# Optimization experiments

Measured on AMD Instinct MI355X. Metric: run time of the kernel, lower is better.

The kernel has to match this reference:

```python
import jax, jax.numpy as jnp
import numpy as np


def _block_causal_mask(cu_seqlens, seq_len):
    """Boolean [seq_len, seq_len] mask: True = attend (same doc AND causal)."""
    positions = jnp.arange(seq_len)
    # searchsorted(side='right') - 1 maps each position to its document id
    seq_ids = jnp.searchsorted(cu_seqlens, positions, side='right') - 1
    same_seq = seq_ids[:, None] == seq_ids[None, :]
    causal = positions[None, :] <= positions[:, None]
    return same_seq & causal


def setup_inputs() -> dict:
    key = jax.random.key(0)
    kq, kk, kv, kc = jax.random.split(key, 4)
    B, H, S, D = 1, 16, 4096, 128
    q = jax.random.normal(kq, (B, H, S, D), dtype=jnp.float32)
    k = jax.random.normal(kk, (B, H, S, D), dtype=jnp.float32)
    v = jax.random.normal(kv, (B, H, S, D), dtype=jnp.float32)
    # 8 packed documents: interior boundaries are sorted random ints in (0, S)
    inner = jnp.sort(jax.random.randint(kc, (7,), 1, S, dtype=jnp.int64))
    cu_seqlens = jnp.concatenate([
        jnp.zeros((1,), jnp.int64), inner, jnp.full((1,), S, jnp.int64)
    ])
    return {"q": q, "k": k, "v": v, "cu_seqlens": cu_seqlens, "max_seqlen": S}


def reference(q, k, v, cu_seqlens, max_seqlen):
    # q, k, v: [B, H, S, D]; block-diagonal causal SDPA over packed sequences.
    S, D = q.shape[2], q.shape[3]
    scale = 1.0 / jnp.sqrt(jnp.asarray(D, q.dtype))
    allow = _block_causal_mask(cu_seqlens, S)  # [S, S] bool
    scores = jnp.einsum('bhsd,bhtd->bhst', q, k) * scale  # [B, H, S, S]
    neg_inf = jnp.asarray(-jnp.inf, scores.dtype)
    scores = jnp.where(allow[None, None], scores, neg_inf)
    probs = jax.nn.softmax(scores, axis=-1)
    return jnp.einsum('bhst,bhtd->bhsd', probs, v)
```

## Files before the change

### kernel.cpp

```cpp
#include <hip/hip_runtime.h>

typedef float  f32x4  __attribute__((ext_vector_type(4)));
typedef __bf16 bf16x8 __attribute__((ext_vector_type(8)));
typedef unsigned short u16;
typedef u16 u16x8 __attribute__((ext_vector_type(8)));
typedef u16 u16x4 __attribute__((ext_vector_type(4)));

#define HEADS 16
#define DIM   128
#define QT    64
#define KTILE 64
#define PSTR  72
#define KSTR  136
#define VSTR  68

__device__ __forceinline__ u16 f2bf(float f) {
    unsigned u = __builtin_bit_cast(unsigned, f);
    u += 0x7FFFu + ((u >> 16) & 1u);
    return (u16)(u >> 16);
}

__device__ __forceinline__ void dma16(const void* g, void* l) {
    auto* gp = (const __attribute__((address_space(1))) unsigned*)(uintptr_t)g;
    auto* lp = (__attribute__((address_space(3))) unsigned*)(uintptr_t)l;
    __builtin_amdgcn_global_load_lds(gp, lp, 16, 0, 0);
}

__global__ __launch_bounds__(256) void prep_k(
    const float* __restrict__ K, u16* __restrict__ KB, int S, int total)
{
    int t = blockIdx.x * 256 + threadIdx.x;
    if (t >= total) return;
    int g = t & 15;
    int k = (t >> 4) % S;
    int h = (t >> 4) / S;
    int r = k & 63, tile = k >> 6;
    const float* src = K + ((long)(h * S + k) * DIM + g * 8);
    f32x4 a = *(const f32x4*)src;
    f32x4 b = *(const f32x4*)(src + 4);
    u16x8 o;
    o[0]=f2bf(a[0]); o[1]=f2bf(a[1]); o[2]=f2bf(a[2]); o[3]=f2bf(a[3]);
    o[4]=f2bf(b[0]); o[5]=f2bf(b[1]); o[6]=f2bf(b[2]); o[7]=f2bf(b[3]);
    long tb = (long)(h * (S >> 6) + tile) * 8192;
    *(u16x8*)&KB[tb + r * 128 + ((g ^ (r & 7)) << 3)] = o;
}

__global__ __launch_bounds__(256) void prep_v(
    const float* __restrict__ V, u16* __restrict__ VB, int S)
{
    __shared__ __align__(16) u16 T[128 * 72];
    int nt = S >> 6;
    int tile = blockIdx.x % nt, h = blockIdx.x / nt;
    int t = threadIdx.x;
    int col4 = (t & 31) * 4;
    int row  = t >> 5;
    const float* src = V + ((long)(h * S + tile * 64)) * DIM;
#pragma unroll
    for (int it = 0; it < 8; ++it) {
        int k = row + it * 8;
        f32x4 x = *(const f32x4*)(src + (long)k * DIM + col4);
        T[(col4 + 0) * 72 + k] = f2bf(x[0]);
        T[(col4 + 1) * 72 + k] = f2bf(x[1]);
        T[(col4 + 2) * 72 + k] = f2bf(x[2]);
        T[(col4 + 3) * 72 + k] = f2bf(x[3]);
    }
    __syncthreads();
    long tb = (long)(h * nt + tile) * 8192;
#pragma unroll
    for (int it = 0; it < 4; ++it) {
        int idx = t + it * 256;
        int d = idx >> 3, g2 = idx & 7;
        u16x8 o = *(const u16x8*)&T[d * 72 + g2 * 8];
        *(u16x8*)&VB[tb + d * 64 + ((g2 ^ (d & 7)) << 3)] = o;
    }
}

__global__ __launch_bounds__(256, 3) void fa_main(
    const float* __restrict__ Q, const u16* __restrict__ KB,
    const u16* __restrict__ VB, const void* __restrict__ cu_raw,
    int n_cu, float* __restrict__ O, int S, int n_qb)
{
    __shared__ __align__(16) u16 Kb[64 * 128];
    __shared__ __align__(16) u16 Vt[144 * 64];
    __shared__ __align__(16) u16 Pw[4][16 * PSTR];
    __shared__ int cu_s[32];

    const int tid  = threadIdx.x;
    const int wave = tid >> 6, lane = tid & 63;
    const int quad = lane >> 4, l16 = lane & 15;
    const int h  = blockIdx.x & (HEADS - 1);
    const int qb = (n_qb - 1) - (blockIdx.x >> 4);
    const int q0 = qb * QT;

    {
        const int* cu32 = (const int*)cu_raw;
        bool is64 = (cu32[1] == 0);
        for (int t = tid; t < n_cu; t += blockDim.x)
            cu_s[t] = is64 ? (int)((const long long*)cu_raw)[t] : cu32[t];
    }
    for (int i = tid; i < 1024; i += 256)
        Vt[8192 + i] = (i < 64) ? (u16)0x3F80 : (u16)0;
    __syncthreads();

    const float sc2 = 0.08838834764831845f * 1.4426950408889634f;
    const long hb = (long)h * S * DIM;
    const long hk = (long)h * (S >> 6) * 8192;
    const int qend = q0 + QT;

    int qstart[4];
#pragma unroll
    for (int r = 0; r < 4; ++r) {
        int qi = q0 + wave * 16 + quad * 4 + r;
        int st = 0;
        for (int j = 0; j < n_cu; ++j) if (cu_s[j] <= qi) st = cu_s[j];
        qstart[r] = st;
    }
    int q0s = 0;
    for (int j = 0; j < n_cu; ++j) if (cu_s[j] <= q0) q0s = cu_s[j];

    bf16x8 qfrag[4];
    {
        const float* qp = Q + hb + (long)(q0 + wave * 16 + l16) * DIM + quad * 8;
#pragma unroll
        for (int kk = 0; kk < 4; ++kk) {
            f32x4 x = *(const f32x4*)(qp + kk * 32);
            f32x4 y = *(const f32x4*)(qp + kk * 32 + 4);
            u16x8 u;
            u[0]=f2bf(x[0]); u[1]=f2bf(x[1]); u[2]=f2bf(x[2]); u[3]=f2bf(x[3]);
            u[4]=f2bf(y[0]); u[5]=f2bf(y[1]); u[6]=f2bf(y[2]); u[7]=f2bf(y[3]);
            qfrag[kk] = __builtin_bit_cast(bf16x8, u);
        }
    }

    f32x4 acc[9];
#pragma unroll
    for (int dt = 0; dt < 9; ++dt) acc[dt] = (f32x4){0.f, 0.f, 0.f, 0.f};

    for (int kt = q0s & ~(KTILE - 1); kt < qend; kt += KTILE) {
        __syncthreads();
        {
            const u16* ks = KB + hk + (long)(kt >> 6) * 8192;
            const u16* vs = VB + hk + (long)(kt >> 6) * 8192;
#pragma unroll
            for (int c = 0; c < 4; ++c) {
                int ch = wave * 4 + c;
                dma16(ks + ch * 512 + lane * 8, &Kb[ch * 512]);
                dma16(vs + ch * 512 + lane * 8, &Vt[ch * 512]);
            }
        }
        __syncthreads();

        f32x4 sc[4];
#pragma unroll
        for (int nt = 0; nt < 4; ++nt) sc[nt] = (f32x4){0.f, 0.f, 0.f, 0.f};
#pragma unroll
        for (int kk = 0; kk < 4; ++kk)
#pragma unroll
            for (int nt = 0; nt < 4; ++nt) {
                int row = nt * 16 + l16;
                int g = kk * 4 + quad;
                u16x8 bu = *(const u16x8*)&Kb[row * 128 + ((g ^ (row & 7)) << 3)];
                sc[nt] = __builtin_amdgcn_mfma_f32_16x16x32_bf16(
                    qfrag[kk], __builtin_bit_cast(bf16x8, bu), sc[nt], 0, 0, 0);
            }

#pragma unroll
        for (int nt = 0; nt < 4; ++nt) {
            int kj = kt + nt * 16 + l16;
#pragma unroll
            for (int r = 0; r < 4; ++r) {
                int qi = q0 + wave * 16 + quad * 4 + r;
                bool ok = (kj >= qstart[r]) && (kj <= qi);
                float pv = ok ? __builtin_amdgcn_exp2f(sc[nt][r] * sc2) : 0.f;
                Pw[wave][(quad*4 + r) * PSTR + ((nt ^ quad) * 16 + l16)] = f2bf(pv);
            }
        }

#pragma unroll
        for (int kk2 = 0; kk2 < 2; ++kk2) {
            int colx = (kk2*32 + quad*8) ^ ((l16 >> 2) << 4);
            u16x8 au = *(const u16x8*)&Pw[wave][l16 * PSTR + colx];
            bf16x8 ap = __builtin_bit_cast(bf16x8, au);
#pragma unroll
            for (int dt = 0; dt < 9; ++dt) {
                int d = dt * 16 + l16;
                int g2 = kk2 * 4 + quad;
                u16x8 bu = *(const u16x8*)&Vt[(d << 6) + ((g2 ^ (d & 7)) << 3)];
                acc[dt] = __builtin_amdgcn_mfma_f32_16x16x32_bf16(
                    ap, __builtin_bit_cast(bf16x8, bu), acc[dt], 0, 0, 0);
            }
        }
    }

#pragma unroll
    for (int r = 0; r < 4; ++r) {
        float l = __shfl(acc[8][r], (lane & 48), 64);
        int qi = q0 + wave * 16 + quad * 4 + r;
        float inv = 1.f / l;
        float* op = O + hb + (long)qi * DIM + l16;
#pragma unroll
        for (int dt = 0; dt < 8; ++dt)
            op[dt * 16] = acc[dt][r] * inv;
    }
}

__global__ __launch_bounds__(256, 2) void fa_fallback(
    const float* __restrict__ Q, const float* __restrict__ K,
    const float* __restrict__ V, const void* __restrict__ cu_raw,
    int n_cu, float* __restrict__ O, int S)
{
    __shared__ __align__(16) u16 Kb[KTILE * KSTR];
    __shared__ __align__(16) u16 Vt[DIM * VSTR];
    __shared__ __align__(16) u16 Pw[4][16 * PSTR];
    __shared__ int cu_s[32];

    const int tid  = threadIdx.x;
    const int wave = tid >> 6, lane = tid & 63;
    const int quad = lane >> 4, l16 = lane & 15;
    const int q0   = blockIdx.x * QT;
    const int h    = blockIdx.y;
    const int cg = tid & 31, rr = tid >> 5;
    const int dv = tid & 127, hiv = tid >> 7;

    {
        const int* cu32 = (const int*)cu_raw;
        bool is64 = (cu32[1] == 0);
        for (int t = tid; t < n_cu; t += blockDim.x)
            cu_s[t] = is64 ? (int)((const long long*)cu_raw)[t] : cu32[t];
    }
    __syncthreads();

    const long hb = (long)h * S * DIM;
    const float NEG_INF = -__builtin_inff();
    const float scale = 0.08838834764831845f;

    int qstart[4];
#pragma unroll
    for (int r = 0; r < 4; ++r) {
        int qi = q0 + wave * 16 + quad * 4 + r;
        int st = 0;
        for (int j = 0; j < n_cu; ++j) if (cu_s[j] <= qi) st = cu_s[j];
        qstart[r] = st;
    }
    int q0s = 0;
    for (int j = 0; j < n_cu; ++j) if (cu_s[j] <= q0) q0s = cu_s[j];

    bf16x8 qfrag[4];
    {
        const float* qp = Q + hb + (long)(q0 + wave * 16 + l16) * DIM + quad * 8;
#pragma unroll
        for (int kk = 0; kk < 4; ++kk) {
            f32x4 x = *(const f32x4*)(qp + kk * 32);
            f32x4 y = *(const f32x4*)(qp + kk * 32 + 4);
            u16x8 u;
            u[0]=f2bf(x[0]); u[1]=f2bf(x[1]); u[2]=f2bf(x[2]); u[3]=f2bf(x[3]);
            u[4]=f2bf(y[0]); u[5]=f2bf(y[1]); u[6]=f2bf(y[2]); u[7]=f2bf(y[3]);
            qfrag[kk] = __builtin_bit_cast(bf16x8, u);
        }
    }

    f32x4 acc[8];
#pragma unroll
    for (int dt = 0; dt < 8; ++dt) acc[dt] = (f32x4){0.f, 0.f, 0.f, 0.f};
    float m_r[4], l_r[4];
#pragma unroll
    for (int r = 0; r < 4; ++r) { m_r[r] = NEG_INF; l_r[r] = 0.f; }

    for (int kt = q0s & ~(KTILE - 1); kt < q0 + QT; kt += KTILE) {
        __syncthreads();
        {
#pragma unroll
            for (int it = 0; it < 8; ++it) {
                f32x4 kx = *(const f32x4*)(K + hb + (long)(kt + rr + it*8) * DIM + cg*4);
                u16x4 kb4;
                kb4[0]=f2bf(kx[0]); kb4[1]=f2bf(kx[1]);
                kb4[2]=f2bf(kx[2]); kb4[3]=f2bf(kx[3]);
                *(u16x4*)&Kb[(rr + it*8) * KSTR + cg*4] = kb4;
            }
#pragma unroll
            for (int p = 0; p < 8; ++p) {
                int kq = 2*p + hiv;
                const float* vp = V + hb + (long)(kt + kq*4) * DIM + dv;
                u16x4 w;
                w[0]=f2bf(vp[0]); w[1]=f2bf(vp[(long)DIM]);
                w[2]=f2bf(vp[(long)2*DIM]); w[3]=f2bf(vp[(long)3*DIM]);
                *(u16x4*)&Vt[dv * VSTR + kq*4] = w;
            }
        }
        __syncthreads();

        f32x4 sc[4];
#pragma unroll
        for (int nt = 0; nt < 4; ++nt) sc[nt] = (f32x4){0.f, 0.f, 0.f, 0.f};
#pragma unroll
        for (int kk = 0; kk < 4; ++kk)
#pragma unroll
            for (int nt = 0; nt < 4; ++nt) {
                u16x8 bu = *(const u16x8*)&Kb[(nt*16 + l16) * KSTR + kk*32 + quad*8];
                sc[nt] = __builtin_amdgcn_mfma_f32_16x16x32_bf16(
                    qfrag[kk], __builtin_bit_cast(bf16x8, bu), sc[nt], 0, 0, 0);
            }
#pragma unroll
        for (int nt = 0; nt < 4; ++nt) {
            int kj = kt + nt * 16 + l16;
#pragma unroll
            for (int r = 0; r < 4; ++r) {
                int qi = q0 + wave * 16 + quad * 4 + r;
                bool ok = (kj >= qstart[r]) && (kj <= qi);
                sc[nt][r] = ok ? sc[nt][r] * scale : NEG_INF;
            }
        }
        float mnew[4], alpha[4], rsum[4];
#pragma unroll
        for (int r = 0; r < 4; ++r) {
            float tm = fmaxf(fmaxf(sc[0][r], sc[1][r]), fmaxf(sc[2][r], sc[3][r]));
#pragma unroll
            for (int off = 1; off < 16; off <<= 1)
                tm = fmaxf(tm, __shfl_xor(tm, off, 64));
            float mn = fmaxf(m_r[r], tm);
            mnew[r]  = mn;
            alpha[r] = (mn == NEG_INF) ? 1.f : __expf(m_r[r] - mn);
            rsum[r]  = 0.f;
        }
#pragma unroll
        for (int nt = 0; nt < 4; ++nt)
#pragma unroll
            for (int r = 0; r < 4; ++r) {
                float pv = (sc[nt][r] == NEG_INF) ? 0.f : __expf(sc[nt][r] - mnew[r]);
                sc[nt][r] = pv;
                rsum[r] += pv;
            }
#pragma unroll
        for (int r = 0; r < 4; ++r) {
            float s = rsum[r];
#pragma unroll
            for (int off = 1; off < 16; off <<= 1) s += __shfl_xor(s, off, 64);
            l_r[r] = l_r[r] * alpha[r] + s;
            m_r[r] = mnew[r];
        }
#pragma unroll
        for (int dt = 0; dt < 8; ++dt)
#pragma unroll
            for (int r = 0; r < 4; ++r) acc[dt][r] *= alpha[r];

#pragma unroll
        for (int nt = 0; nt < 4; ++nt)
#pragma unroll
            for (int r = 0; r < 4; ++r)
                Pw[wave][(quad*4 + r) * PSTR + ((nt ^ quad) * 16 + l16)] = f2bf(sc[nt][r]);

#pragma unroll
        for (int kk2 = 0; kk2 < 2; ++kk2) {
            int colx = (kk2*32 + quad*8) ^ ((l16 >> 2) << 4);
            u16x8 au = *(const u16x8*)&Pw[wave][l16 * PSTR + colx];
            bf16x8 ap = __builtin_bit_cast(bf16x8, au);
#pragma unroll
            for (int dt = 0; dt < 8; ++dt) {
                int base = (dt*16 + l16) * VSTR + kk2*32 + quad*8;
                u16x4 lo = *(const u16x4*)&Vt[base];
                u16x4 hi = *(const u16x4*)&Vt[base + 4];
                u16x8 bu;
                bu[0]=lo[0]; bu[1]=lo[1]; bu[2]=lo[2]; bu[3]=lo[3];
                bu[4]=hi[0]; bu[5]=hi[1]; bu[6]=hi[2]; bu[7]=hi[3];
                acc[dt] = __builtin_amdgcn_mfma_f32_16x16x32_bf16(
                    ap, __builtin_bit_cast(bf16x8, bu), acc[dt], 0, 0, 0);
            }
        }
    }

#pragma unroll
    for (int r = 0; r < 4; ++r) {
        int qi = q0 + wave * 16 + quad * 4 + r;
        float inv = 1.f / l_r[r];
        float* op = O + hb + (long)qi * DIM + l16;
#pragma unroll
        for (int dt = 0; dt < 8; ++dt)
            op[dt * 16] = acc[dt][r] * inv;
    }
}

extern "C" void kernel_launch(void* const* d_in, const int* in_sizes, int n_in,
                              void* d_out, int out_size, void* d_ws, size_t ws_size,
                              hipStream_t stream) {
    const float* q = (const float*)d_in[0];
    const float* k = (const float*)d_in[1];
    const float* v = (const float*)d_in[2];
    const void* cu = d_in[3];
    int n_cu = in_sizes[3];
    int S = in_sizes[0] / (HEADS * DIM);
    size_t perMat = (size_t)HEADS * S * 256;
    if (ws_size >= 2 * perMat) {
        u16* KB = (u16*)d_ws;
        u16* VB = (u16*)((char*)d_ws + perMat);
        int totalK = HEADS * S * 16;
        prep_k<<<dim3((totalK + 255) / 256), 256, 0, stream>>>(k, KB, S, totalK);
        prep_v<<<dim3(HEADS * (S >> 6)), 256, 0, stream>>>(v, VB, S);
        int n_qb = S / QT;
        fa_main<<<dim3(n_qb * HEADS), 256, 0, stream>>>(
            q, KB, VB, cu, n_cu, (float*)d_out, S, n_qb);
    } else {
        fa_fallback<<<dim3(S / QT, HEADS), 256, 0, stream>>>(
            q, k, v, cu, n_cu, (float*)d_out, S);
    }
}
```

Measured before the change: 187.3 us.

## Double-buffer K/V tiles with async LDS prefetch and merge K/V prep kernels

The attention kernel now keeps two K/V tile buffers in shared memory and issues the direct-to-LDS loads for the next tile before computing the current one. It waits with explicit vmcnt counts and raw barriers in place of two __syncthreads per tile, and raises wave priority around the MFMA sections. The ones-row used to accumulate the softmax denominator moves to its own small LDS buffer, and the separate K and V bf16 conversion kernels are merged into one launch. The larger LDS footprint lowers the occupancy hint from 3 to 2 blocks per CU, which could offset the gain from overlapping loads with compute.

New measurement: 186.6 us. About the same (-0.4%).

```diff
diff --git a/kernel.cpp b/kernel.cpp
--- a/kernel.cpp
+++ b/kernel.cpp
@@ -26,46 +26,43 @@
     __builtin_amdgcn_global_load_lds(gp, lp, 16, 0, 0);
 }
 
-__global__ __launch_bounds__(256) void prep_k(
-    const float* __restrict__ K, u16* __restrict__ KB, int S, int total)
-{
-    int t = blockIdx.x * 256 + threadIdx.x;
-    if (t >= total) return;
-    int g = t & 15;
-    int k = (t >> 4) % S;
-    int h = (t >> 4) / S;
-    int r = k & 63, tile = k >> 6;
-    const float* src = K + ((long)(h * S + k) * DIM + g * 8);
-    f32x4 a = *(const f32x4*)src;
-    f32x4 b = *(const f32x4*)(src + 4);
-    u16x8 o;
-    o[0]=f2bf(a[0]); o[1]=f2bf(a[1]); o[2]=f2bf(a[2]); o[3]=f2bf(a[3]);
-    o[4]=f2bf(b[0]); o[5]=f2bf(b[1]); o[6]=f2bf(b[2]); o[7]=f2bf(b[3]);
-    long tb = (long)(h * (S >> 6) + tile) * 8192;
-    *(u16x8*)&KB[tb + r * 128 + ((g ^ (r & 7)) << 3)] = o;
-}
-
-__global__ __launch_bounds__(256) void prep_v(
-    const float* __restrict__ V, u16* __restrict__ VB, int S)
+__global__ __launch_bounds__(256) void prep_kv(
+    const float* __restrict__ K, const float* __restrict__ V,
+    u16* __restrict__ KB, u16* __restrict__ VB, int S)
 {
     __shared__ __align__(16) u16 T[128 * 72];
     int nt = S >> 6;
     int tile = blockIdx.x % nt, h = blockIdx.x / nt;
     int t = threadIdx.x;
+    long tb = (long)(h * nt + tile) * 8192;
+
+    const float* ksrc = K + ((long)(h * S + tile * 64)) * DIM;
+#pragma unroll
+    for (int it = 0; it < 4; ++it) {
+        int idx = t + it * 256;
+        int g = idx & 15, r = idx >> 4;
+        const float* src = ksrc + (long)r * DIM + g * 8;
+        f32x4 a = *(const f32x4*)src;
+        f32x4 b = *(const f32x4*)(src + 4);
+        u16x8 o;
+        o[0]=f2bf(a[0]); o[1]=f2bf(a[1]); o[2]=f2bf(a[2]); o[3]=f2bf(a[3]);
+        o[4]=f2bf(b[0]); o[5]=f2bf(b[1]); o[6]=f2bf(b[2]); o[7]=f2bf(b[3]);
+        *(u16x8*)&KB[tb + r * 128 + ((g ^ (r & 7)) << 3)] = o;
+    }
+
     int col4 = (t & 31) * 4;
     int row  = t >> 5;
-    const float* src = V + ((long)(h * S + tile * 64)) * DIM;
+    const float* vsrc = V + ((long)(h * S + tile * 64)) * DIM;
 #pragma unroll
     for (int it = 0; it < 8; ++it) {
         int k = row + it * 8;
-        f32x4 x = *(const f32x4*)(src + (long)k * DIM + col4);
+        f32x4 x = *(const f32x4*)(vsrc + (long)k * DIM + col4);
         T[(col4 + 0) * 72 + k] = f2bf(x[0]);
         T[(col4 + 1) * 72 + k] = f2bf(x[1]);
         T[(col4 + 2) * 72 + k] = f2bf(x[2]);
         T[(col4 + 3) * 72 + k] = f2bf(x[3]);
     }
     __syncthreads();
-    long tb = (long)(h * nt + tile) * 8192;
 #pragma unroll
     for (int it = 0; it < 4; ++it) {
         int idx = t + it * 256;
@@ -75,13 +72,14 @@
     }
 }
 
-__global__ __launch_bounds__(256, 3) void fa_main(
+__global__ __launch_bounds__(256, 2) void fa_main(
     const float* __restrict__ Q, const u16* __restrict__ KB,
     const u16* __restrict__ VB, const void* __restrict__ cu_raw,
     int n_cu, float* __restrict__ O, int S, int n_qb)
 {
-    __shared__ __align__(16) u16 Kb[64 * 128];
-    __shared__ __align__(16) u16 Vt[144 * 64];
+    __shared__ __align__(16) u16 Kb[2][64 * 128];
+    __shared__ __align__(16) u16 Vt[2][128 * 64];
+    __shared__ __align__(16) u16 On[16 * 64];
     __shared__ __align__(16) u16 Pw[4][16 * PSTR];
     __shared__ int cu_s[32];
 
@@ -99,7 +97,7 @@
             cu_s[t] = is64 ? (int)((const long long*)cu_raw)[t] : cu32[t];
     }
     for (int i = tid; i < 1024; i += 256)
-        Vt[8192 + i] = (i < 64) ? (u16)0x3F80 : (u16)0;
+        On[i] = (i < 64) ? (u16)0x3F80 : (u16)0;
     __syncthreads();
 
     const float sc2 = 0.08838834764831845f * 1.4426950408889634f;
@@ -136,33 +134,56 @@
 #pragma unroll
     for (int dt = 0; dt < 9; ++dt) acc[dt] = (f32x4){0.f, 0.f, 0.f, 0.f};
 
-    for (int kt = q0s & ~(KTILE - 1); kt < qend; kt += KTILE) {
-        __syncthreads();
-        {
-            const u16* ks = KB + hk + (long)(kt >> 6) * 8192;
-            const u16* vs = VB + hk + (long)(kt >> 6) * 8192;
+    const int t0 = (q0s & ~(KTILE - 1)) >> 6;
+    const int ntile = (qend >> 6) - t0;
+    const u16* ksrc = KB + hk;
+    const u16* vsrc = VB + hk;
+
+    {
+        long off = (long)t0 * 8192;
+#pragma unroll
+        for (int c = 0; c < 4; ++c) {
+            int ch = wave * 4 + c;
+            dma16(ksrc + off + ch * 512 + lane * 8, &Kb[0][ch * 512]);
+            dma16(vsrc + off + ch * 512 + lane * 8, &Vt[0][ch * 512]);
+        }
+    }
+
+    for (int i = 0; i < ntile; ++i) {
+        const int cur = i & 1;
+        if (i + 1 < ntile) {
+            long off = (long)(t0 + i + 1) * 8192;
 #pragma unroll
             for (int c = 0; c < 4; ++c) {
                 int ch = wave * 4 + c;
-                dma16(ks + ch * 512 + lane * 8, &Kb[ch * 512]);
-                dma16(vs + ch * 512 + lane * 8, &Vt[ch * 512]);
-            }
-        }
-        __syncthreads();
+                dma16(ksrc + off + ch * 512 + lane * 8, &Kb[cur ^ 1][ch * 512]);
+                dma16(vsrc + off + ch * 512 + lane * 8, &Vt[cur ^ 1][ch * 512]);
+            }
+            asm volatile("s_waitcnt vmcnt(8)" ::: "memory");
+        } else {
+            asm volatile("s_waitcnt vmcnt(0)" ::: "memory");
+        }
+        __builtin_amdgcn_s_barrier();
+
+        const int kt = (t0 + i) << 6;
+        const u16* kb = &Kb[cur][0];
+        const u16* vt = &Vt[cur][0];
 
         f32x4 sc[4];
 #pragma unroll
         for (int nt = 0; nt < 4; ++nt) sc[nt] = (f32x4){0.f, 0.f, 0.f, 0.f};
+        __builtin_amdgcn_s_setprio(1);
 #pragma unroll
         for (int kk = 0; kk < 4; ++kk)
 #pragma unroll
             for (int nt = 0; nt < 4; ++nt) {
                 int row = nt * 16 + l16;
                 int g = kk * 4 + quad;
-                u16x8 bu = *(const u16x8*)&Kb[row * 128 + ((g ^ (row & 7)) << 3)];
+                u16x8 bu = *(const u16x8*)&kb[row * 128 + ((g ^ (row & 7)) << 3)];
                 sc[nt] = __builtin_amdgcn_mfma_f32_16x16x32_bf16(
                     qfrag[kk], __builtin_bit_cast(bf16x8, bu), sc[nt], 0, 0, 0);
             }
+        __builtin_amdgcn_s_setprio(0);
 
 #pragma unroll
         for (int nt = 0; nt < 4; ++nt) {
@@ -176,20 +197,29 @@
             }
         }
 
+        __builtin_amdgcn_s_setprio(1);
 #pragma unroll
         for (int kk2 = 0; kk2 < 2; ++kk2) {
             int colx = (kk2*32 + quad*8) ^ ((l16 >> 2) << 4);
             u16x8 au = *(const u16x8*)&Pw[wave][l16 * PSTR + colx];
             bf16x8 ap = __builtin_bit_cast(bf16x8, au);
-#pragma unroll
-            for (int dt = 0; dt < 9; ++dt) {
+            int g2 = kk2 * 4 + quad;
+#pragma unroll
+            for (int dt = 0; dt < 8; ++dt) {
                 int d = dt * 16 + l16;
-                int g2 = kk2 * 4 + quad;
-                u16x8 bu = *(const u16x8*)&Vt[(d << 6) + ((g2 ^ (d & 7)) << 3)];
+                u16x8 bu = *(const u16x8*)&vt[(d << 6) + ((g2 ^ (d & 7)) << 3)];
                 acc[dt] = __builtin_amdgcn_mfma_f32_16x16x32_bf16(
                     ap, __builtin_bit_cast(bf16x8, bu), acc[dt], 0, 0, 0);
             }
-        }
+            {
+                u16x8 bo = *(const u16x8*)&On[(l16 << 6) + ((g2 ^ (l16 & 7)) << 3)];
+                acc[8] = __builtin_amdgcn_mfma_f32_16x16x32_bf16(
+                    ap, __builtin_bit_cast(bf16x8, bo), acc[8], 0, 0, 0);
+            }
+        }
+        __builtin_amdgcn_s_setprio(0);
+
+        __builtin_amdgcn_s_barrier();
     }
 
 #pragma unroll
@@ -392,9 +422,7 @@
     if (ws_size >= 2 * perMat) {
         u16* KB = (u16*)d_ws;
         u16* VB = (u16*)((char*)d_ws + perMat);
-        int totalK = HEADS * S * 16;
-        prep_k<<<dim3((totalK + 255) / 256), 256, 0, stream>>>(k, KB, S, totalK);
-        prep_v<<<dim3(HEADS * (S >> 6)), 256, 0, stream>>>(v, VB, S);
+        prep_kv<<<dim3(HEADS * (S >> 6)), 256, 0, stream>>>(k, v, KB, VB, S);
         int n_qb = S / QT;
         fa_main<<<dim3(n_qb * HEADS), 256, 0, stream>>>(
             q, KB, VB, cu, n_cu, (float*)d_out, S, n_qb);
```
